# Performance work log

Hardware: AMD Instinct MI355X
Metric: run time of the kernel (lower is better)

The kernel has to match this reference:

```python
import jax, jax.numpy as jnp
import numpy as np
from jax import lax


def _dct_basis():
    # 64 separable 2D DCT-II basis filters, shape [64,1,8,8] (OIHW)
    k = 8
    a = np.full(k, np.sqrt(2.0 / k)); a[0] = np.sqrt(1.0 / k)
    u = np.arange(k)[:, None]; xx = np.arange(k)[None, :]
    B = a[:, None] * np.cos((2 * xx + 1) * u * np.pi / (2 * k))  # [u, x]
    basis = np.einsum('ux,vy->uvxy', B, B).reshape(64, 1, k, k)
    return jnp.asarray(basis, dtype=jnp.float32)


def _conv(x, w, b, pad):
    y = lax.conv_general_dilated(x, w, (1, 1), [(pad, pad), (pad, pad)],
                                 dimension_numbers=('NCHW', 'OIHW', 'NCHW'))
    return y + b[None, :, None, None]


def _bn(x, s, b, m, v, eps=1e-5):
    inv = s * lax.rsqrt(v + eps)
    return x * inv[None, :, None, None] + (b - m * inv)[None, :, None, None]


def _mp2(x):
    return lax.reduce_window(x, -jnp.inf, lax.max, (1, 1, 2, 2), (1, 1, 2, 2), 'VALID')


def setup_inputs() -> dict:
    key = jax.random.key(0)
    ks = jax.random.split(key, 32)
    B = 128
    d = {}
    d['x'] = jax.random.normal(ks[0], (B, 1, 256, 256), jnp.float32)
    d['qvectors'] = jax.random.uniform(ks[1], (B, 64), jnp.float32)
    d['dct_basis'] = _dct_basis()
    def w(k, shape, sc=0.02):
        return jax.random.normal(k, shape, jnp.float32) * sc
    # conv stack
    d['conv1a_w'] = w(ks[2], (64, 1, 5, 5));   d['conv1a_b'] = w(ks[3], (64,))
    d['conv1b_w'] = w(ks[4], (64, 64, 5, 5));  d['conv1b_b'] = w(ks[5], (64,))
    d['conv2a_w'] = w(ks[6], (128, 64, 5, 5)); d['conv2a_b'] = w(ks[7], (128,))
    d['conv3a_w'] = w(ks[8], (256, 128, 5, 5)); d['conv3a_b'] = w(ks[9], (256,))
    # batchnorm (eval-mode) params: scale, bias, running_mean, running_var
    for i, (name, c) in enumerate([('bn1a', 64), ('bn1b', 64), ('bn2a', 128), ('bn3a', 256)]):
        kk = jax.random.split(ks[10 + i], 4)
        d[name + '_s'] = 1.0 + w(kk[0], (c,))
        d[name + '_b'] = w(kk[1], (c,))
        d[name + '_m'] = w(kk[2], (c,))
        d[name + '_v'] = jax.random.uniform(kk[3], (c,), jnp.float32, 0.5, 1.5)
    d['fc1_w'] = w(ks[20], (500, 15 * 8 * 256 + 64), 0.01); d['fc1_b'] = w(ks[21], (500,))
    d['fc2_w'] = w(ks[22], (500, 564), 0.01);               d['fc2_b'] = w(ks[23], (500,))
    d['fc3_w'] = w(ks[24], (2, 564), 0.01);                 d['fc3_b'] = w(ks[25], (2,))
    return d


def reference(x, qvectors, dct_basis,
              conv1a_w, conv1a_b, bn1a_s, bn1a_b, bn1a_m, bn1a_v,
              conv1b_w, conv1b_b, bn1b_s, bn1b_b, bn1b_m, bn1b_v,
              conv2a_w, conv2a_b, bn2a_s, bn2a_b, bn2a_m, bn2a_v,
              conv3a_w, conv3a_b, bn3a_s, bn3a_b, bn3a_m, bn3a_v,
              fc1_w, fc1_b, fc2_w, fc2_b, fc3_w, fc3_b):
    gamma = 1e6
    # --- soft-histogram over DCT coefficients (no_grad in the original) ---
    dct = lax.conv_general_dilated(x, dct_basis, (8, 8), 'VALID',
                                   dimension_numbers=('NCHW', 'OIHW', 'NCHW'))  # [B,64,32,32]
    bins = jnp.arange(-60, 61, dtype=jnp.float32)  # 121 bins

    def step(_, b):
        s = jnp.sum(jax.nn.sigmoid(gamma * (dct - b)), axis=(2, 3)) / 1024.0  # [B,64]
        return None, s
    _, feats = lax.scan(step, None, bins)           # [121,B,64]
    feats = jnp.transpose(feats, (1, 0, 2))          # [B,121,64]
    features = feats[:, 0:120, :] - feats[:, 1:121, :]
    features = lax.stop_gradient(features.reshape(-1, 1, 120, 64))

    # --- CNN backbone ---
    h = jax.nn.relu(_bn(_conv(features, conv1a_w, conv1a_b, 2), bn1a_s, bn1a_b, bn1a_m, bn1a_v))
    h = jax.nn.relu(_bn(_conv(h, conv1b_w, conv1b_b, 2), bn1b_s, bn1b_b, bn1b_m, bn1b_v))
    h = _mp2(h)
    h = jax.nn.relu(_bn(_conv(h, conv2a_w, conv2a_b, 2), bn2a_s, bn2a_b, bn2a_m, bn2a_v))
    h = _mp2(h)
    h = jax.nn.relu(_bn(_conv(h, conv3a_w, conv3a_b, 2), bn3a_s, bn3a_b, bn3a_m, bn3a_v))
    h = _mp2(h)                                      # [B,256,15,8]
    h_flat = h.reshape(-1, 15 * 8 * 256)
    h = jnp.concatenate([qvectors, h_flat], axis=1)
    h = jax.nn.relu(h @ fc1_w.T + fc1_b)
    h = jnp.concatenate([qvectors, h], axis=1)
    h = jax.nn.relu(h @ fc2_w.T + fc2_b)
    h = jnp.concatenate([qvectors, h], axis=1)
    return h @ fc3_w.T + fc3_b
```

## Files before the change

kernel.cpp:

```cpp
#include <hip/hip_runtime.h>


typedef _Float16 half8 __attribute__((ext_vector_type(8)));
typedef _Float16 half4 __attribute__((ext_vector_type(4)));
typedef float f32x16 __attribute__((ext_vector_type(16)));

__device__ __forceinline__ void async_copy16(const void* g, void* l) {
  __builtin_amdgcn_global_load_lds(
      (__attribute__((address_space(1))) void*)g,
      (__attribute__((address_space(3))) void*)l, 16, 0, 0);
}

__global__ __launch_bounds__(256) void dcthist_kernel(const float* __restrict__ x,
                                                      const float* __restrict__ basis,
                                                      float* __restrict__ feat) {
  __shared__ __align__(16) float Bm[64];
  __shared__ float Hl[128 * 121];
  int tid = threadIdx.x;
  if (tid < 64) {
    int u = tid >> 3, xx = tid & 7;
    Bm[tid] = basis[(u * 8) * 64 + xx * 8] * 2.8284271247461903f;
  }
  for (int i = tid; i < 128 * 121; i += 256) Hl[i] = 0.f;
  __syncthreads();
  int gb = blockIdx.x;
  int b = gb >> 2;
  int blk = (gb & 3) * 256 + tid;
  int bi = blk >> 5, bj = blk & 31;
  const float* xp = x + (size_t)b * 65536 + (bi * 8) * 256 + bj * 8;
  float X[64];
#pragma unroll
  for (int r = 0; r < 8; ++r) {
    float4 p = *(const float4*)(xp + r * 256);
    float4 q = *(const float4*)(xp + r * 256 + 4);
    X[r * 8 + 0] = p.x; X[r * 8 + 1] = p.y; X[r * 8 + 2] = p.z; X[r * 8 + 3] = p.w;
    X[r * 8 + 4] = q.x; X[r * 8 + 5] = q.y; X[r * 8 + 6] = q.z; X[r * 8 + 7] = q.w;
  }
  float T[64];
#pragma unroll
  for (int u = 0; u < 8; ++u) {
    float t[8] = {0.f, 0.f, 0.f, 0.f, 0.f, 0.f, 0.f, 0.f};
#pragma unroll
    for (int xx = 0; xx < 8; ++xx) {
      float bm = Bm[u * 8 + xx];
#pragma unroll
      for (int y = 0; y < 8; ++y) t[y] += bm * X[xx * 8 + y];
    }
#pragma unroll
    for (int y = 0; y < 8; ++y) T[u * 8 + y] = t[y];
  }
  int vr = tid & 7;
  int sub = (tid >> 3) & 1;
#pragma unroll 1
  for (int vv = 0; vv < 8; ++vv) {
    int v = (vv + vr) & 7;
    float dc[8] = {0.f, 0.f, 0.f, 0.f, 0.f, 0.f, 0.f, 0.f};
#pragma unroll
    for (int y = 0; y < 8; ++y) {
      float bm = Bm[v * 8 + y];
#pragma unroll
      for (int u = 0; u < 8; ++u) dc[u] += bm * T[u * 8 + y];
    }
#pragma unroll
    for (int u = 0; u < 8; ++u) {
      float d = dc[u];
      float* hc = Hl + ((u * 8 + v) * 2 + sub) * 121;
      float fl = floorf(d);
      float t0 = d - fl;
      int k = (int)fl + 60;
      if (t0 >= 2e-5f && t0 <= 1.f - 1.2e-4f) {
        if (k >= 0 && k < 120) atomicAdd(hc + k, 1.0f);
      } else {
        float s0 = 1.f / (1.f + expf(-1e6f * t0));
        float s1 = 1.f / (1.f + expf(1e6f * (1.f - t0)));
        if (k >= 1 && k <= 120) atomicAdd(hc + k - 1, 1.f - s0);
        if (k >= 0 && k < 120)  atomicAdd(hc + k, s0 - s1);
        if (k >= -1 && k < 119) atomicAdd(hc + k + 1, s1);
      }
    }
  }
  __syncthreads();
  float* fb = feat + (size_t)b * 7680;
  for (int i = tid; i < 7680; i += 256) {
    int f = i >> 6, c = i & 63;
    atomicAdd(fb + i, Hl[(c * 2) * 121 + f] + Hl[(c * 2 + 1) * 121 + f]);
  }
}

template <int CI, int CO>
__global__ __launch_bounds__(256) void wtrans(const float* __restrict__ w,
                                              _Float16* __restrict__ wt) {
  int i = blockIdx.x * 256 + threadIdx.x;
  if (i >= (CI / 8) * 26 * CO * 8) return;
  int c8 = i & 7;
  int t = i >> 3;
  int co = t % CO; t /= CO;
  int k = t % 26;
  int cg = t / 26;
  int ci = cg * 8 + c8;
  float v = (k < 25) ? w[((size_t)co * CI + ci) * 25 + k] : 0.f;
  wt[i] = (_Float16)v;
}

__global__ __launch_bounds__(512) void bnprep3(
    const float* __restrict__ cb1, const float* __restrict__ s1,
    const float* __restrict__ b1, const float* __restrict__ m1,
    const float* __restrict__ v1, float* __restrict__ sc1, float* __restrict__ sh1,
    const float* __restrict__ cb2, const float* __restrict__ s2,
    const float* __restrict__ b2, const float* __restrict__ m2,
    const float* __restrict__ v2, float* __restrict__ sc2, float* __restrict__ sh2,
    const float* __restrict__ cb3, const float* __restrict__ s3,
    const float* __restrict__ b3, const float* __restrict__ m3,
    const float* __restrict__ v3, float* __restrict__ sc3, float* __restrict__ sh3) {
  int i = threadIdx.x;
  if (i < 64) {
    float inv = s1[i] * rsqrtf(v1[i] + 1e-5f);
    sc1[i] = inv;
    sh1[i] = (cb1[i] - m1[i]) * inv + b1[i];
  } else if (i < 192) {
    int j = i - 64;
    float inv = s2[j] * rsqrtf(v2[j] + 1e-5f);
    sc2[j] = inv;
    sh2[j] = (cb2[j] - m2[j]) * inv + b2[j];
  } else if (i < 448) {
    int j = i - 192;
    float inv = s3[j] * rsqrtf(v3[j] + 1e-5f);
    sc3[j] = inv;
    sh3[j] = (cb3[j] - m3[j]) * inv + b3[j];
  }
}

__global__ __launch_bounds__(256) void conv1a_f16(
    const float* __restrict__ in, const float* __restrict__ wts,
    const float* __restrict__ cb, const float* __restrict__ s_,
    const float* __restrict__ b_, const float* __restrict__ m_,
    const float* __restrict__ v_, _Float16* __restrict__ out) {
  __shared__ __align__(16) float wl[5 * 8 * 20];
  __shared__ __align__(16) float il[12 * 68];
  int tid = threadIdx.x, bid = blockIdx.x;
  int img = bid / 30;
  int r = bid % 30;
  int cob = r / 15;
  int h0 = (r % 15) * 8;
  int cog = tid & 7, wg = (tid >> 3) & 3, hh = tid >> 5;
  float acc[4][16];
#pragma unroll
  for (int i = 0; i < 4; ++i)
#pragma unroll
    for (int j = 0; j < 16; ++j) acc[i][j] = 0.f;
  for (int idx = tid; idx < 32 * 25; idx += 256) {
    int rr = idx % 25, co = idx / 25;
    float v = wts[(cob * 32 + co) * 25 + rr] * (1.f / 1024.f);
    int kh = rr / 5, kw = rr % 5;
    wl[(kh * 8 + (co >> 2)) * 20 + (co & 3) * 5 + kw] = v;
  }
  for (int idx = tid; idx < 12 * 68; idx += 256) {
    int cc = idx % 68, rr = idx / 68;
    int hy = h0 + rr - 2, wx = cc - 2;
    float v = 0.f;
    if (hy >= 0 && hy < 120 && wx >= 0 && wx < 64)
      v = in[(size_t)img * 7680 + hy * 64 + wx];
    il[idx] = v;
  }
  __syncthreads();
#pragma unroll
  for (int kh = 0; kh < 5; ++kh) {
    const float* ir = &il[(hh + kh) * 68 + wg * 16];
    float iv[20];
#pragma unroll
    for (int i = 0; i < 5; ++i) {
      float4 p = *(const float4*)(ir + i * 4);
      iv[i * 4] = p.x; iv[i * 4 + 1] = p.y; iv[i * 4 + 2] = p.z; iv[i * 4 + 3] = p.w;
    }
    const float* wr = &wl[(kh * 8 + cog) * 20];
    float wv[20];
#pragma unroll
    for (int i = 0; i < 5; ++i) {
      float4 p = *(const float4*)(wr + i * 4);
      wv[i * 4] = p.x; wv[i * 4 + 1] = p.y; wv[i * 4 + 2] = p.z; wv[i * 4 + 3] = p.w;
    }
#pragma unroll
    for (int co = 0; co < 4; ++co)
#pragma unroll
      for (int kw = 0; kw < 5; ++kw) {
        float w1 = wv[co * 5 + kw];
#pragma unroll
        for (int w = 0; w < 16; ++w) acc[co][w] += w1 * iv[w + kw];
      }
  }
  int h = h0 + hh;
  int co0 = cob * 32 + cog * 4;
  float inv[4], bia[4];
#pragma unroll
  for (int i = 0; i < 4; ++i) {
    int c = co0 + i;
    inv[i] = s_[c] * rsqrtf(v_[c] + 1e-5f);
    bia[i] = (cb[c] - m_[c]) * inv[i] + b_[c];
  }
  int g = co0 >> 3, off = co0 & 7;
  _Float16* op = out + (((size_t)(img * 8 + g) * 120 + h) * 64) * 8 + off;
#pragma unroll
  for (int w = 0; w < 16; ++w) {
    half4 o;
#pragma unroll
    for (int i = 0; i < 4; ++i)
      o[i] = (_Float16)fmaxf(acc[i][w] * inv[i] + bia[i], 0.f);
    *(half4*)&op[(size_t)(wg * 16 + w) * 8] = o;
  }
}

template <int CI, int CO, int H, int W, int BLK_M, bool OUT_NCHW, bool DBUF>
__global__ __launch_bounds__(512) void conv5_mfma(
    const _Float16* __restrict__ in, const _Float16* __restrict__ wt,
    const float* __restrict__ scale, const float* __restrict__ shift,
    _Float16* __restrict__ out) {
  constexpr int NW_M = BLK_M / 64;
  constexpr int NW_N = 8 / NW_M;
  constexpr int BLK_N = NW_N * 128;
  constexpr int ROWS = BLK_N / W;
  constexpr int TB = (H + ROWS - 1) / ROWS;
  constexpr int NCOB = CO / BLK_M;
  constexpr int HR = ROWS + 4;
  constexpr int HC = W + 4;
  constexpr int CIG = CI / 8;
  constexpr int OH = H / 2, OW = W / 2;
  constexpr int AITER = (HR * HC + 511) / 512;
  constexpr int WBYTES = 26 * BLK_M * 16;
  constexpr int WITER = (WBYTES + 8191) / 8192;
  constexpr int NBUF = DBUF ? 2 : 1;
  constexpr int ASZ = HR * HC * 8;
  constexpr int WSZ = 26 * BLK_M * 8;
  __shared__ __align__(16) _Float16 Alds[NBUF][ASZ];
  __shared__ __align__(16) _Float16 Wlds[NBUF][WSZ];

  int tid = threadIdx.x;
  int bid = blockIdx.x;
  int img = bid / (TB * NCOB);
  int r = bid % (TB * NCOB);
  int tb = r / NCOB;
  int cob = r % NCOB;
  int h0 = tb * ROWS;

  int wid = tid >> 6, l = tid & 63, lo = l & 31, hi = l >> 5;
  int widM = wid / NW_N, widN = wid % NW_N;

  int wbase[2];
#pragma unroll
  for (int mi = 0; mi < 2; ++mi)
    wbase[mi] = (hi * BLK_M + widM * 64 + mi * 32 + lo) * 8;
  int bbase[4];
#pragma unroll
  for (int j = 0; j < 4; ++j) {
    int pix = widN * 128 + j * 32 + lo;
    bbase[j] = ((pix / W) * HC + (pix % W)) * 8;
  }

  f32x16 acc[2][4];
#pragma unroll
  for (int mi = 0; mi < 2; ++mi)
#pragma unroll
    for (int j = 0; j < 4; ++j) acc[mi][j] = (f32x16){};

  auto loadA = [&](int cg, half8* areg) {
    const _Float16* ing = in + (size_t)(img * CIG + cg) * H * W * 8;
#pragma unroll
    for (int it = 0; it < AITER; ++it) {
      int i = tid + it * 512;
      half8 v = {};
      if (i < HR * HC) {
        int rr = i / HC, cc = i % HC;
        int hy = h0 + rr - 2, wx = cc - 2;
        if (hy >= 0 && hy < H && wx >= 0 && wx < W)
          v = *(const half8*)&ing[(size_t)(hy * W + wx) * 8];
      }
      areg[it] = v;
    }
  };
  auto issueW = [&](int cg, int buf) {
    const char* wsrc = (const char*)(wt + ((size_t)cg * 26 * CO + cob * BLK_M) * 8);
#pragma unroll
    for (int rr = 0; rr < WITER; ++rr) {
      int f = rr * 8192 + tid * 16;
      if (f < WBYTES) {
        int row = f / (BLK_M * 16);
        int off = f % (BLK_M * 16);
        async_copy16(wsrc + (size_t)row * (CO * 16) + off,
                     (char*)&Wlds[buf][0] + (rr * 8192 + wid * 1024));
      }
    }
  };
  auto writeA = [&](int buf, half8* areg) {
#pragma unroll
    for (int it = 0; it < AITER; ++it) {
      int i = tid + it * 512;
      if (i < HR * HC) *(half8*)&Alds[buf][i * 8] = areg[it];
    }
  };
  auto ldfrag = [&](int buf, int p, half8 (&af)[2], half8 (&bf)[4]) {
    int pos0 = 2 * p, pos1 = 2 * p + 1;
    int off0 = (pos0 / 5) * HC + (pos0 % 5);
    int off1 = (pos1 < 25) ? (pos1 / 5) * HC + (pos1 % 5) : 0;
    int off = (hi ? off1 : off0) * 8;
#pragma unroll
    for (int mi = 0; mi < 2; ++mi)
      af[mi] = *(const half8*)&Wlds[buf][wbase[mi] + pos0 * BLK_M * 8];
#pragma unroll
    for (int j = 0; j < 4; ++j)
      bf[j] = *(const half8*)&Alds[buf][bbase[j] + off];
  };
  auto compute = [&](int buf) {
    half8 afA[2], bfA[4], afB[2], bfB[4];
    ldfrag(buf, 0, afA, bfA);
#pragma unroll
    for (int p = 0; p < 13; ++p) {
      const bool even = (p & 1) == 0;
      if (p + 1 < 13) {
        if (even) ldfrag(buf, p + 1, afB, bfB);
        else      ldfrag(buf, p + 1, afA, bfA);
      }
      __builtin_amdgcn_s_setprio(1);
#pragma unroll
      for (int mi = 0; mi < 2; ++mi)
#pragma unroll
        for (int j = 0; j < 4; ++j)
          acc[mi][j] = __builtin_amdgcn_mfma_f32_32x32x16_f16(
              even ? afA[mi] : afB[mi], even ? bfA[j] : bfB[j],
              acc[mi][j], 0, 0, 0);
      __builtin_amdgcn_s_setprio(0);
    }
  };

  if constexpr (DBUF) {
    half8 areg[AITER];
    loadA(0, areg);
    issueW(0, 0);
    writeA(0, areg);
    __syncthreads();
#pragma unroll 1
    for (int cg = 0; cg < CIG; ++cg) {
      int cur = cg & 1;
      if (cg + 1 < CIG) {
        loadA(cg + 1, areg);
        issueW(cg + 1, cur ^ 1);
      }
      compute(cur);
      if (cg + 1 < CIG) writeA(cur ^ 1, areg);
      __syncthreads();
    }
  } else {
#pragma unroll 1
    for (int cg = 0; cg < CIG; ++cg) {
      half8 areg[AITER];
      loadA(cg, areg);
      issueW(cg, 0);
      writeA(0, areg);
      __syncthreads();
      compute(0);
      __syncthreads();
    }
  }

  if (!OUT_NCHW) {
    constexpr int CGO = CO / 8;
    int gbase = (cob * BLK_M + widM * 64) >> 3;
    bool lane_ok = ((lo & 1) == 0);
#pragma unroll
    for (int mi = 0; mi < 2; ++mi) {
#pragma unroll
      for (int r4 = 0; r4 < 4; ++r4) {
        int g = gbase + mi * 4 + r4;
        int co0 = g * 8 + hi * 4;
        float4 sv = *(const float4*)&scale[co0];
        float4 tv = *(const float4*)&shift[co0];
        float sa[4] = {sv.x, sv.y, sv.z, sv.w};
        float ta[4] = {tv.x, tv.y, tv.z, tv.w};
#pragma unroll
        for (int p = 0; p < 2; ++p) {
          int ja = (W == 64) ? p : 2 * p;
          int jb = (W == 64) ? p + 2 : 2 * p + 1;
          int orow = (W == 64) ? (h0 >> 1) + widN : (h0 >> 1) + widN * 2 + p;
          int ocol = (W == 64) ? p * 16 + (lo >> 1) : (lo >> 1);
          half4 o;
#pragma unroll
          for (int c = 0; c < 4; ++c) {
            int reg = r4 * 4 + c;
            float v0 = fmaxf(acc[mi][ja][reg] * sa[c] + ta[c], 0.f);
            float v1 = fmaxf(acc[mi][jb][reg] * sa[c] + ta[c], 0.f);
            float m = fmaxf(v0, v1);
            m = fmaxf(m, __shfl_xor(m, 1, 64));
            o[c] = (_Float16)m;
          }
          if (lane_ok && orow < OH)
            *(half4*)&out[(((size_t)(img * CGO + g) * OH + orow) * OW + ocol) * 8 +
                          hi * 4] = o;
        }
      }
    }
  } else {
    bool lane_ok = ((lo & 1) == 0) && (lo < 16);
#pragma unroll
    for (int mi = 0; mi < 2; ++mi) {
#pragma unroll
      for (int reg = 0; reg < 16; ++reg) {
        int co = cob * BLK_M + widM * 64 + mi * 32 + (reg & 3) + 8 * (reg >> 2) + 4 * hi;
        float s = scale[co], t = shift[co];
#pragma unroll
        for (int j = 0; j < 4; ++j) {
          float v = fmaxf(acc[mi][j][reg] * s + t, 0.f);
          float m = fmaxf(v, __shfl_xor(v, 16, 64));
          m = fmaxf(m, __shfl_xor(m, 1, 64));
          int orow = (h0 >> 1) + widN * 4 + j;
          if (lane_ok && orow < OH)
            out[((size_t)(img * CO + co) * OH + orow) * OW + ((lo & 15) >> 1)] =
                (_Float16)m;
        }
      }
    }
  }
}

__global__ __launch_bounds__(256, 2) void fc1_mfma(const float* __restrict__ qv,
                                                   const _Float16* __restrict__ p3,
                                                   const float* __restrict__ w,
                                                   float* __restrict__ part) {
  __shared__ __align__(16) _Float16 Wl[8 * 256 * 8];
  __shared__ __align__(16) _Float16 Bl[8 * 128 * 8];
  int tid = threadIdx.x;
  int ks = blockIdx.x >> 1, mt = blockIdx.x & 1;
  int wid = tid >> 6, l = tid & 63, lo = l & 31, hi = l >> 5;
  f32x16 acc[2][4];
#pragma unroll
  for (int mi = 0; mi < 2; ++mi)
#pragma unroll
    for (int j = 0; j < 4; ++j) acc[mi][j] = (f32x16){};

#pragma unroll 1
  for (int i3 = 0; i3 < 5; ++i3) {
    int c = ks + 120 * i3;
    if (c > 480) break;
    for (int idx = tid; idx < 2048; idx += 256) {
      int n_loc = idx >> 3, k8 = idx & 7;
      int n = mt * 256 + n_loc;
      half8 v = {};
      if (n < 500) {
        const float* src = w + (size_t)n * 30784 + c * 64 + k8 * 8;
        float4 f0 = *(const float4*)src;
        float4 f1 = *(const float4*)(src + 4);
        v[0] = (_Float16)f0.x; v[1] = (_Float16)f0.y;
        v[2] = (_Float16)f0.z; v[3] = (_Float16)f0.w;
        v[4] = (_Float16)f1.x; v[5] = (_Float16)f1.y;
        v[6] = (_Float16)f1.z; v[7] = (_Float16)f1.w;
      }
      *(half8*)&Wl[(size_t)(k8 * 256 + n_loc) * 8] = v;
    }
    for (int idx = tid; idx < 1024; idx += 256) {
      int img = idx >> 3, k8 = idx & 7;
      half8 v;
      if (c == 0) {
        const float* src = qv + img * 64 + k8 * 8;
        float4 f0 = *(const float4*)src;
        float4 f1 = *(const float4*)(src + 4);
        v[0] = (_Float16)f0.x; v[1] = (_Float16)f0.y;
        v[2] = (_Float16)f0.z; v[3] = (_Float16)f0.w;
        v[4] = (_Float16)f1.x; v[5] = (_Float16)f1.y;
        v[6] = (_Float16)f1.z; v[7] = (_Float16)f1.w;
      } else {
        v = *(const half8*)&p3[(size_t)img * 30720 + (c * 64 - 64) + k8 * 8];
      }
      *(half8*)&Bl[(size_t)(k8 * 128 + img) * 8] = v;
    }
    __syncthreads();
#pragma unroll
    for (int ks16 = 0; ks16 < 4; ++ks16) {
      half8 af[2], bf[4];
#pragma unroll
      for (int mi = 0; mi < 2; ++mi)
        af[mi] = *(const half8*)&Wl[(size_t)((ks16 * 2 + hi) * 256 + wid * 64 +
                                             mi * 32 + lo) * 8];
#pragma unroll
      for (int j = 0; j < 4; ++j)
        bf[j] = *(const half8*)&Bl[(size_t)((ks16 * 2 + hi) * 128 + j * 32 + lo) * 8];
#pragma unroll
      for (int mi = 0; mi < 2; ++mi)
#pragma unroll
        for (int j = 0; j < 4; ++j)
          acc[mi][j] = __builtin_amdgcn_mfma_f32_32x32x16_f16(
              af[mi], bf[j], acc[mi][j], 0, 0, 0);
    }
    __syncthreads();
  }
#pragma unroll
  for (int mi = 0; mi < 2; ++mi)
#pragma unroll
    for (int reg = 0; reg < 16; ++reg) {
      int n = mt * 256 + wid * 64 + mi * 32 + (reg & 3) + 8 * (reg >> 2) + 4 * hi;
#pragma unroll
      for (int j = 0; j < 4; ++j)
        part[((size_t)ks * 512 + n) * 128 + j * 32 + lo] = acc[mi][j][reg];
    }
}

__global__ __launch_bounds__(256) void fc1_reduce(const float* __restrict__ part,
                                                  const float* __restrict__ bias,
                                                  float* __restrict__ out) {
  int idx = blockIdx.x * 256 + threadIdx.x;
  int img = idx & 127, n = idx >> 7;
  float s = 0.f;
#pragma unroll 8
  for (int ks = 0; ks < 120; ++ks) s += part[((size_t)ks * 512 + n) * 128 + img];
  out[n * 128 + img] = (n < 500) ? fmaxf(s + bias[n], 0.f) : 0.f;
}

__global__ __launch_bounds__(256) void fc2_kernel(const float* __restrict__ qv,
                                                  const float* __restrict__ fc1o,
                                                  const float* __restrict__ w,
                                                  const float* __restrict__ bias,
                                                  float* __restrict__ out) {
  int idx = blockIdx.x * 256 + threadIdx.x;
  if (idx >= 128 * 500) return;
  int m = idx & 127, n = idx >> 7;
  const float* wr = w + (size_t)n * 564;
  float acc = 0.f;
#pragma unroll 8
  for (int k = 0; k < 64; ++k) acc += qv[m * 64 + k] * wr[k];
#pragma unroll 4
  for (int k = 0; k < 500; ++k) acc += fc1o[k * 128 + m] * wr[64 + k];
  out[n * 128 + m] = fmaxf(acc + bias[n], 0.f);
}

__global__ __launch_bounds__(256) void fc3_kernel(const float* __restrict__ qv,
                                                  const float* __restrict__ fc2o,
                                                  const float* __restrict__ w,
                                                  const float* __restrict__ bias,
                                                  float* __restrict__ out) {
  int tid = threadIdx.x;
  int m = tid >> 1, n = tid & 1;
  const float* wr = w + (size_t)n * 564;
  float acc = 0.f;
#pragma unroll 8
  for (int k = 0; k < 64; ++k) acc += qv[m * 64 + k] * wr[k];
#pragma unroll 4
  for (int k = 0; k < 500; ++k) acc += fc2o[k * 128 + m] * wr[64 + k];
  out[m * 2 + n] = acc + bias[n];
}

extern "C" void kernel_launch(void* const* d_in, const int* in_sizes, int n_in,
                              void* d_out, int out_size, void* d_ws, size_t ws_size,
                              hipStream_t stream) {
  (void)in_sizes; (void)n_in; (void)out_size; (void)ws_size;
  const float* x      = (const float*)d_in[0];
  const float* qv     = (const float*)d_in[1];
  const float* basis  = (const float*)d_in[2];
  const float* c1aw   = (const float*)d_in[3];
  const float* c1ab   = (const float*)d_in[4];
  const float* c1bw   = (const float*)d_in[5];
  const float* c1bb   = (const float*)d_in[6];
  const float* c2aw   = (const float*)d_in[7];
  const float* c2ab   = (const float*)d_in[8];
  const float* c3aw   = (const float*)d_in[9];
  const float* c3ab   = (const float*)d_in[10];
  const float* bn1a_s = (const float*)d_in[11];
  const float* bn1a_b = (const float*)d_in[12];
  const float* bn1a_m = (const float*)d_in[13];
  const float* bn1a_v = (const float*)d_in[14];
  const float* bn1b_s = (const float*)d_in[15];
  const float* bn1b_b = (const float*)d_in[16];
  const float* bn1b_m = (const float*)d_in[17];
  const float* bn1b_v = (const float*)d_in[18];
  const float* bn2a_s = (const float*)d_in[19];
  const float* bn2a_b = (const float*)d_in[20];
  const float* bn2a_m = (const float*)d_in[21];
  const float* bn2a_v = (const float*)d_in[22];
  const float* bn3a_s = (const float*)d_in[23];
  const float* bn3a_b = (const float*)d_in[24];
  const float* bn3a_m = (const float*)d_in[25];
  const float* bn3a_v = (const float*)d_in[26];
  const float* fc1w   = (const float*)d_in[27];
  const float* fc1b   = (const float*)d_in[28];
  const float* fc2w   = (const float*)d_in[29];
  const float* fc2b   = (const float*)d_in[30];
  const float* fc3w   = (const float*)d_in[31];
  const float* fc3b   = (const float*)d_in[32];

  float* ws = (float*)d_ws;
  float* feat = ws;
  _Float16* wt1b = (_Float16*)(ws + 1000000);
  _Float16* wt2a = (_Float16*)(ws + 1070000);
  _Float16* wt3a = (_Float16*)(ws + 1200000);
  float* sc1b = ws + 1700000; float* sh1b = ws + 1700100;
  float* sc2a = ws + 1700200; float* sh2a = ws + 1700400;
  float* sc3a = ws + 1700600; float* sh3a = ws + 1701000;
  _Float16* p1 = (_Float16*)(ws + 1710000);
  float* S = ws + 9600000;
  _Float16* a1c  = (_Float16*)S;
  _Float16* p2   = (_Float16*)(ws + 25400000);
  _Float16* p3   = (_Float16*)(ws + 1710000);
  float* f1p  = S;
  float* f1o  = ws + 29400000;
  float* f2o  = ws + 29500000;

  wtrans<64, 64><<<416, 256, 0, stream>>>(c1bw, wt1b);
  wtrans<64, 128><<<832, 256, 0, stream>>>(c2aw, wt2a);
  wtrans<128, 256><<<3328, 256, 0, stream>>>(c3aw, wt3a);
  bnprep3<<<1, 512, 0, stream>>>(c1bb, bn1b_s, bn1b_b, bn1b_m, bn1b_v, sc1b, sh1b,
                                 c2ab, bn2a_s, bn2a_b, bn2a_m, bn2a_v, sc2a, sh2a,
                                 c3ab, bn3a_s, bn3a_b, bn3a_m, bn3a_v, sc3a, sh3a);

  hipMemsetAsync(feat, 0, 983040 * sizeof(float), stream);
  dcthist_kernel<<<512, 256, 0, stream>>>(x, basis, feat);

  for (int c = 0; c < 2; ++c) {
    const float* fin = feat + (size_t)c * 64 * 120 * 64;
    _Float16* pout = p1 + (size_t)c * 64 * 8 * 60 * 32 * 8;
    conv1a_f16<<<64 * 30, 256, 0, stream>>>(fin, c1aw, c1ab, bn1a_s, bn1a_b,
                                            bn1a_m, bn1a_v, a1c);
    conv5_mfma<64, 64, 120, 64, 64, false, false><<<64 * 8, 512, 0, stream>>>(
        a1c, wt1b, sc1b, sh1b, pout);
  }

  conv5_mfma<64, 128, 60, 32, 128, false, false><<<128 * 4, 512, 0, stream>>>(
      p1, wt2a, sc2a, sh2a, p2);

  conv5_mfma<128, 256, 30, 16, 128, true, false><<<128 * 2, 512, 0, stream>>>(
      p2, wt3a, sc3a, sh3a, p3);

  fc1_mfma<<<240, 256, 0, stream>>>(qv, p3, fc1w, f1p);
  fc1_reduce<<<256, 256, 0, stream>>>(f1p, fc1b, f1o);
  fc2_kernel<<<250, 256, 0, stream>>>(qv, f1o, fc2w, fc2b, f2o);
  fc3_kernel<<<1, 256, 0, stream>>>(qv, f2o, fc3w, fc3b, (float*)d_out);
}
```

Baseline: 763.7 us.

## Run conv2a/conv3a with 256-thread blocks and four M-tiles per wave

Makes the thread count a template parameter of the conv5_mfma kernel. conv2a and conv3a now launch with 256 threads (4 waves), and each wave owns the full 128-channel M block (MI=4), so every A fragment feeds more MFMAs. The change also removes the unused double-buffer path and adds a min-blocks=2 launch bound for 512-thread configs to limit register use. The trade-off is fewer waves per block available to hide latency, and the 4-wave path drops the software-pipelined fragment prefetch.

```diff
diff --git a/kernel.cpp b/kernel.cpp
--- a/kernel.cpp
+++ b/kernel.cpp
@@ -209,13 +209,15 @@
   }
 }
 
-template <int CI, int CO, int H, int W, int BLK_M, bool OUT_NCHW, bool DBUF>
-__global__ __launch_bounds__(512) void conv5_mfma(
+template <int CI, int CO, int H, int W, int BLK_M, int THREADS, bool OUT_NCHW>
+__global__ __launch_bounds__(THREADS, (THREADS == 512) ? 2 : 1) void conv5_mfma(
     const _Float16* __restrict__ in, const _Float16* __restrict__ wt,
     const float* __restrict__ scale, const float* __restrict__ shift,
     _Float16* __restrict__ out) {
-  constexpr int NW_M = BLK_M / 64;
-  constexpr int NW_N = 8 / NW_M;
+  constexpr int WAVES = THREADS / 64;
+  constexpr int NW_M = (WAVES == 8) ? (BLK_M / 64) : 1;
+  constexpr int NW_N = WAVES / NW_M;
+  constexpr int MI = BLK_M / (NW_M * 32);
   constexpr int BLK_N = NW_N * 128;
   constexpr int ROWS = BLK_N / W;
   constexpr int TB = (H + ROWS - 1) / ROWS;
@@ -224,14 +226,13 @@
   constexpr int HC = W + 4;
   constexpr int CIG = CI / 8;
   constexpr int OH = H / 2, OW = W / 2;
-  constexpr int AITER = (HR * HC + 511) / 512;
+  constexpr int AITER = (HR * HC + THREADS - 1) / THREADS;
   constexpr int WBYTES = 26 * BLK_M * 16;
-  constexpr int WITER = (WBYTES + 8191) / 8192;
-  constexpr int NBUF = DBUF ? 2 : 1;
+  constexpr int WITER = (WBYTES + THREADS * 16 - 1) / (THREADS * 16);
   constexpr int ASZ = HR * HC * 8;
   constexpr int WSZ = 26 * BLK_M * 8;
-  __shared__ __align__(16) _Float16 Alds[NBUF][ASZ];
-  __shared__ __align__(16) _Float16 Wlds[NBUF][WSZ];
+  __shared__ __align__(16) _Float16 Alds[ASZ];
+  __shared__ __align__(16) _Float16 Wlds[WSZ];
 
   int tid = threadIdx.x;
   int bid = blockIdx.x;
@@ -244,10 +245,10 @@
   int wid = tid >> 6, l = tid & 63, lo = l & 31, hi = l >> 5;
   int widM = wid / NW_N, widN = wid % NW_N;
 
-  int wbase[2];
-#pragma unroll
-  for (int mi = 0; mi < 2; ++mi)
-    wbase[mi] = (hi * BLK_M + widM * 64 + mi * 32 + lo) * 8;
+  int wbase[MI];
+#pragma unroll
+  for (int mi = 0; mi < MI; ++mi)
+    wbase[mi] = (hi * BLK_M + widM * (MI * 32) + mi * 32 + lo) * 8;
   int bbase[4];
 #pragma unroll
   for (int j = 0; j < 4; ++j) {
@@ -255,9 +256,9 @@
     bbase[j] = ((pix / W) * HC + (pix % W)) * 8;
   }
 
-  f32x16 acc[2][4];
-#pragma unroll
-  for (int mi = 0; mi < 2; ++mi)
+  f32x16 acc[MI][4];
+#pragma unroll
+  for (int mi = 0; mi < MI; ++mi)
 #pragma unroll
     for (int j = 0; j < 4; ++j) acc[mi][j] = (f32x16){};
 
@@ -265,7 +266,7 @@
     const _Float16* ing = in + (size_t)(img * CIG + cg) * H * W * 8;
 #pragma unroll
     for (int it = 0; it < AITER; ++it) {
-      int i = tid + it * 512;
+      int i = tid + it * THREADS;
       half8 v = {};
       if (i < HR * HC) {
         int rr = i / HC, cc = i % HC;
@@ -276,96 +277,94 @@
       areg[it] = v;
     }
   };
-  auto issueW = [&](int cg, int buf) {
+  auto issueW = [&](int cg) {
     const char* wsrc = (const char*)(wt + ((size_t)cg * 26 * CO + cob * BLK_M) * 8);
 #pragma unroll
     for (int rr = 0; rr < WITER; ++rr) {
-      int f = rr * 8192 + tid * 16;
+      int f = rr * (THREADS * 16) + tid * 16;
       if (f < WBYTES) {
         int row = f / (BLK_M * 16);
         int off = f % (BLK_M * 16);
         async_copy16(wsrc + (size_t)row * (CO * 16) + off,
-                     (char*)&Wlds[buf][0] + (rr * 8192 + wid * 1024));
+                     (char*)Wlds + (rr * (THREADS * 16) + wid * 1024));
       }
     }
   };
-  auto writeA = [&](int buf, half8* areg) {
+  auto writeA = [&](half8* areg) {
 #pragma unroll
     for (int it = 0; it < AITER; ++it) {
-      int i = tid + it * 512;
-      if (i < HR * HC) *(half8*)&Alds[buf][i * 8] = areg[it];
+      int i = tid + it * THREADS;
+      if (i < HR * HC) *(half8*)&Alds[i * 8] = areg[it];
     }
   };
-  auto ldfrag = [&](int buf, int p, half8 (&af)[2], half8 (&bf)[4]) {
+  auto ldfrag = [&](int p, half8 (&af)[MI], half8 (&bf)[4]) {
     int pos0 = 2 * p, pos1 = 2 * p + 1;
     int off0 = (pos0 / 5) * HC + (pos0 % 5);
     int off1 = (pos1 < 25) ? (pos1 / 5) * HC + (pos1 % 5) : 0;
     int off = (hi ? off1 : off0) * 8;
 #pragma unroll
-    for (int mi = 0; mi < 2; ++mi)
-      af[mi] = *(const half8*)&Wlds[buf][wbase[mi] + pos0 * BLK_M * 8];
+    for (int mi = 0; mi < MI; ++mi)
+      af[mi] = *(const half8*)&Wlds[wbase[mi] + pos0 * BLK_M * 8];
 #pragma unroll
     for (int j = 0; j < 4; ++j)
-      bf[j] = *(const half8*)&Alds[buf][bbase[j] + off];
+      bf[j] = *(const half8*)&Alds[bbase[j] + off];
   };
-  auto compute = [&](int buf) {
-    half8 afA[2], bfA[4], afB[2], bfB[4];
-    ldfrag(buf, 0, afA, bfA);
-#pragma unroll
-    for (int p = 0; p < 13; ++p) {
-      const bool even = (p & 1) == 0;
-      if (p + 1 < 13) {
-        if (even) ldfrag(buf, p + 1, afB, bfB);
-        else      ldfrag(buf, p + 1, afA, bfA);
-      }
-      __builtin_amdgcn_s_setprio(1);
-#pragma unroll
-      for (int mi = 0; mi < 2; ++mi)
-#pragma unroll
-        for (int j = 0; j < 4; ++j)
-          acc[mi][j] = __builtin_amdgcn_mfma_f32_32x32x16_f16(
-              even ? afA[mi] : afB[mi], even ? bfA[j] : bfB[j],
-              acc[mi][j], 0, 0, 0);
-      __builtin_amdgcn_s_setprio(0);
-    }
+  auto mfmaMI = [&](half8 (&af)[MI], half8 (&bf)[4]) {
+#pragma unroll
+    for (int mi = 0; mi < MI; ++mi)
+#pragma unroll
+      for (int j = 0; j < 4; ++j)
+        acc[mi][j] = __builtin_amdgcn_mfma_f32_32x32x16_f16(
+            af[mi], bf[j], acc[mi][j], 0, 0, 0);
   };
-
-  if constexpr (DBUF) {
+  auto compute = [&]() {
+    if constexpr (WAVES == 8) {
+      half8 afA[MI], bfA[4], afB[MI], bfB[4];
+      ldfrag(0, afA, bfA);
+#pragma unroll
+      for (int p = 0; p < 13; ++p) {
+        const bool even = (p & 1) == 0;
+        if (p + 1 < 13) {
+          if (even) ldfrag(p + 1, afB, bfB);
+          else      ldfrag(p + 1, afA, bfA);
+        }
+        __builtin_amdgcn_s_setprio(1);
+#pragma unroll
+        for (int mi = 0; mi < MI; ++mi)
+#pragma unroll
+          for (int j = 0; j < 4; ++j)
+            acc[mi][j] = __builtin_amdgcn_mfma_f32_32x32x16_f16(
+                even ? afA[mi] : afB[mi], even ? bfA[j] : bfB[j],
+                acc[mi][j], 0, 0, 0);
+        __builtin_amdgcn_s_setprio(0);
+      }
+    } else {
+#pragma unroll
+      for (int p = 0; p < 13; ++p) {
+        half8 af[MI], bf[4];
+        ldfrag(p, af, bf);
+        mfmaMI(af, bf);
+      }
+    }
+  };
+
+#pragma unroll 1
+  for (int cg = 0; cg < CIG; ++cg) {
     half8 areg[AITER];
-    loadA(0, areg);
-    issueW(0, 0);
-    writeA(0, areg);
+    loadA(cg, areg);
+    issueW(cg);
+    writeA(areg);
     __syncthreads();
-#pragma unroll 1
-    for (int cg = 0; cg < CIG; ++cg) {
-      int cur = cg & 1;
-      if (cg + 1 < CIG) {
-        loadA(cg + 1, areg);
-        issueW(cg + 1, cur ^ 1);
-      }
-      compute(cur);
-      if (cg + 1 < CIG) writeA(cur ^ 1, areg);
-      __syncthreads();
-    }
-  } else {
-#pragma unroll 1
-    for (int cg = 0; cg < CIG; ++cg) {
-      half8 areg[AITER];
-      loadA(cg, areg);
-      issueW(cg, 0);
-      writeA(0, areg);
-      __syncthreads();
-      compute(0);
-      __syncthreads();
-    }
+    compute();
+    __syncthreads();
   }
 
   if (!OUT_NCHW) {
     constexpr int CGO = CO / 8;
-    int gbase = (cob * BLK_M + widM * 64) >> 3;
+    int gbase = (cob * BLK_M + widM * (MI * 32)) >> 3;
     bool lane_ok = ((lo & 1) == 0);
 #pragma unroll
-    for (int mi = 0; mi < 2; ++mi) {
+    for (int mi = 0; mi < MI; ++mi) {
 #pragma unroll
       for (int r4 = 0; r4 < 4; ++r4) {
         int g = gbase + mi * 4 + r4;
@@ -399,10 +398,11 @@
   } else {
     bool lane_ok = ((lo & 1) == 0) && (lo < 16);
 #pragma unroll
-    for (int mi = 0; mi < 2; ++mi) {
+    for (int mi = 0; mi < MI; ++mi) {
 #pragma unroll
       for (int reg = 0; reg < 16; ++reg) {
-        int co = cob * BLK_M + widM * 64 + mi * 32 + (reg & 3) + 8 * (reg >> 2) + 4 * hi;
+        int co = cob * BLK_M + widM * (MI * 32) + mi * 32 + (reg & 3) +
+                 8 * (reg >> 2) + 4 * hi;
         float s = scale[co], t = shift[co];
 #pragma unroll
         for (int j = 0; j < 4; ++j) {
@@ -614,14 +614,14 @@
     _Float16* pout = p1 + (size_t)c * 64 * 8 * 60 * 32 * 8;
     conv1a_f16<<<64 * 30, 256, 0, stream>>>(fin, c1aw, c1ab, bn1a_s, bn1a_b,
                                             bn1a_m, bn1a_v, a1c);
-    conv5_mfma<64, 64, 120, 64, 64, false, false><<<64 * 8, 512, 0, stream>>>(
+    conv5_mfma<64, 64, 120, 64, 64, 512, false><<<64 * 8, 512, 0, stream>>>(
         a1c, wt1b, sc1b, sh1b, pout);
   }
 
-  conv5_mfma<64, 128, 60, 32, 128, false, false><<<128 * 4, 512, 0, stream>>>(
+  conv5_mfma<64, 128, 60, 32, 128, 256, false><<<128 * 4, 256, 0, stream>>>(
       p1, wt2a, sc2a, sh2a, p2);
 
-  conv5_mfma<128, 256, 30, 16, 128, true, false><<<128 * 2, 512, 0, stream>>>(
+  conv5_mfma<128, 256, 30, 16, 128, 256, true><<<128 * 2, 256, 0, stream>>>(
       p2, wt3a, sc3a, sh3a, p3);
 
   fc1_mfma<<<240, 256, 0, stream>>>(qv, p3, fc1w, f1p);
```

After: 1.030 ms. +34.9%, slower.
